# Kernel tuning notes

Measured on AMD Instinct MI355X. Metric: run time of the kernel, lower is better.

Reference implementation:

```python
import jax, jax.numpy as jnp
from jax import lax
import numpy as np

# --- module hyperparams (match S2_GaussianBlur(nr=2048, nc=2048, kernelSize=10, scale=2, RealData=False)) ---
NR, NC, KS, SCALE = 2048, 2048, 10, 2
MTF = np.array([0.38, 0.34, 0.34, 0.26, 0.22, 0.23])  # mtf[[4,5,6,8,10,11]] for scale==2
C = len(MTF)


def _gaussian_kernels():
    # sigmas = scale * sqrt(-2 ln(mtf) / pi^2)
    sigmas = SCALE * np.sqrt(-2.0 * np.log(MTF) / np.pi ** 2)  # (C,)
    end = int(KS / 2) - 0.5
    coords = np.arange(-end, end + 1.0, 1.0)  # (KS,) = [-4.5, ..., 4.5]
    g1 = np.exp(-coords[None, :] ** 2 / (2.0 * sigmas[:, None] ** 2)) / (
        sigmas[:, None] * np.sqrt(2.0 * np.pi))  # (C,KS)
    k = g1[:, :, None] * g1[:, None, :]  # separable outer product -> (C,KS,KS)
    k = k / k.sum(axis=(1, 2), keepdims=True)
    return k.astype(np.float32)


_KERNELS = jnp.asarray(_gaussian_kernels())  # (C,KS,KS), fixed buffers (requires_grad=False)

# Offsets replicating: circular pad by (nr//2, nc//2), conv with full-image kernel B
# (Gaussian patch placed at [row_start:row_end, col_start:col_end], then flipped both
# axes), crop [0:-1, 0:-1].  This collapses exactly to a circular cross-correlation
# with the flipped KSxKS patch at a fixed shift:
_MIDL, _MIDC = NR // 2, NC // 2
_EB = -int(SCALE / 2)
_ROW_START = int(_MIDL - KS / 2 + _EB)
_COL_START = int(_MIDC - KS / 2 + _EB)
_PAD_T = _MIDL + _ROW_START + KS - NR  # left/top circular pad (=4 here)
_PAD_L = _MIDC + _COL_START + KS - NC
assert 0 <= _PAD_T < KS and 0 <= _PAD_L < KS


def setup_inputs() -> dict:
    key = jax.random.key(0)
    x = jax.random.normal(key, (1, C, NR, NC), dtype=jnp.float32)
    return {"x": x}


def _blur(x):
    # circular (wrap) pad so every output pixel sees its KSxKS circular neighborhood
    xpad = jnp.pad(x, ((0, 0), (0, 0), (_PAD_T, KS - 1 - _PAD_T), (_PAD_L, KS - 1 - _PAD_L)), mode="wrap")
    # flipped Gaussian patch (the full-image kernel B was flipped on both axes)
    w = _KERNELS[:, ::-1, ::-1][:, None, :, :]  # (C,1,KS,KS), depthwise
    return lax.conv_general_dilated(
        xpad, w, window_strides=(1, 1), padding="VALID",
        dimension_numbers=("NCHW", "OIHW", "NCHW"), feature_group_count=C)


def reference(x):
    return _blur(x)  # (1,C,NR,NC)
```

## Files before the change

### kernel.cpp

```cpp
#include <hip/hip_runtime.h>
#include <math.h>

constexpr int C   = 6;
constexpr int NR  = 2048;
constexpr int NC  = 2048;
constexpr int KS  = 10;
constexpr int PAD = 4;

constexpr int R    = 32;
constexpr int NIT  = R + KS - 1;
constexpr int CPT  = 4;
constexpr int BW   = 256 * CPT;

__device__ __constant__ float MTFf[C] = {0.38f, 0.34f, 0.34f, 0.26f, 0.22f, 0.23f};

__global__ __launch_bounds__(256, 3)
void s2_blur_ring(const float* __restrict__ x, float* __restrict__ out)
{
    const int t  = threadIdx.x;
    const int c  = blockIdx.z;
    const int r0 = blockIdx.y * R;
    const int jt = blockIdx.x * BW + t * CPT;

    const float* xc = x   + (size_t)c * NR * NC;
    float*       oc = out + (size_t)c * NR * NC;

    float w[KS];
    {
        float mtf    = MTFf[c];
        float sig    = 2.0f * sqrtf(-2.0f * logf(mtf) / (float)(M_PI * M_PI));
        float inv2s2 = 1.0f / (2.0f * sig * sig);
        float s = 0.0f;
        #pragma unroll
        for (int d = 0; d < KS; ++d) {
            float cd = -4.5f + (float)d;
            w[d] = expf(-cd * cd * inv2s2);
            s += w[d];
        }
        #pragma unroll
        for (int d = 0; d < KS; ++d) w[d] /= s;
    }

    const int off0 = (jt - PAD +  0 + NC) & (NC - 1);
    const int off1 = (jt - PAD +  4 + NC) & (NC - 1);
    const int off2 = (jt - PAD +  8 + NC) & (NC - 1);
    const int off3 = (jt - PAD + 12 + NC) & (NC - 1);

    float acc[KS][CPT];
    #pragma unroll
    for (int s = 0; s < KS; ++s)
        #pragma unroll
        for (int q = 0; q < CPT; ++q) acc[s][q] = 0.0f;

    float4 f0, f1, f2, f3;
    {
        const float* rp = xc + (size_t)((r0 - PAD + NR) & (NR - 1)) * NC;
        f0 = *(const float4*)(rp + off0);
        f1 = *(const float4*)(rp + off1);
        f2 = *(const float4*)(rp + off2);
        f3 = *(const float4*)(rp + off3);
    }

    #pragma unroll
    for (int k = 0; k < NIT; ++k) {
        float4 g0, g1, g2, g3;
        if (k + 1 < NIT) {
            const float* rp = xc + (size_t)((r0 - PAD + k + 1) & (NR - 1)) * NC;
            g0 = *(const float4*)(rp + off0);
            g1 = *(const float4*)(rp + off1);
            g2 = *(const float4*)(rp + off2);
            g3 = *(const float4*)(rp + off3);
        }

        const float f[16] = {f0.x, f0.y, f0.z, f0.w,
                             f1.x, f1.y, f1.z, f1.w,
                             f2.x, f2.y, f2.z, f2.w,
                             f3.x, f3.y, f3.z, f3.w};
        float H[CPT];
        #pragma unroll
        for (int q = 0; q < CPT; ++q) {
            float a = 0.0f;
            #pragma unroll
            for (int d = 0; d < KS; ++d) a = fmaf(w[d], f[q + d], a);
            H[q] = a;
        }

        #pragma unroll
        for (int o = 0; o < KS; ++o) {
            const int m = k - o;
            if (m >= 0 && m < R) {
                const int s = m % KS;
                #pragma unroll
                for (int q = 0; q < CPT; ++q)
                    acc[s][q] = fmaf(w[o], H[q], acc[s][q]);
            }
        }

        if (k >= KS - 1) {
            const int m = k - (KS - 1);
            const int s = m % KS;
            float* orow = oc + (size_t)(r0 + m) * NC;
            *(float4*)(orow + jt) = make_float4(acc[s][0], acc[s][1], acc[s][2], acc[s][3]);
            #pragma unroll
            for (int q = 0; q < CPT; ++q) acc[s][q] = 0.0f;
        }

        f0 = g0; f1 = g1; f2 = g2; f3 = g3;
    }
}

extern "C" void kernel_launch(void* const* d_in, const int* in_sizes, int n_in,
                              void* d_out, int out_size, void* d_ws, size_t ws_size,
                              hipStream_t stream) {
    const float* x = (const float*)d_in[0];
    float* out = (float*)d_out;
    dim3 grid(NC / BW, NR / R, C);
    dim3 block(256);
    s2_blur_ring<<<grid, block, 0, stream>>>(x, out);
}
```

Baseline: 183.4 us.

## Stage input rows through LDS with async global_load_lds ring buffer

Replaces the four overlapping per-thread float4 global loads per row with two direct global-to-LDS async loads per lane. Each wave gets its own 4-deep LDS ring of rows, prefetched three rows ahead, and explicit s_waitcnt vmcnt waits gate each read. The loop is fully unrolled with compile-time indices so the wait counts and accumulator slots are constants. The aim is fewer redundant vector-memory instructions and fewer prefetch registers. In exchange it adds LDS traffic, and because vmcnt also counts stores, the hand-counted waits may end up more conservative than intended.

```diff
diff --git a/kernel.cpp b/kernel.cpp
--- a/kernel.cpp
+++ b/kernel.cpp
@@ -7,20 +7,37 @@
 constexpr int KS  = 10;
 constexpr int PAD = 4;
 
-constexpr int R    = 32;
-constexpr int NIT  = R + KS - 1;
-constexpr int CPT  = 4;
-constexpr int BW   = 256 * CPT;
+constexpr int R     = 32;
+constexpr int NIT   = R + KS - 1;
+constexpr int CPT   = 4;
+constexpr int BW    = 256 * CPT;
+constexpr int DEPTH = 4;
+constexpr int WROW  = 272;
 
 __device__ __constant__ float MTFf[C] = {0.38f, 0.34f, 0.34f, 0.26f, 0.22f, 0.23f};
 
+template<int K> struct IC { static constexpr int v = K; };
+template<int K, int N, typename F>
+__device__ __forceinline__ void static_for(F&& f) {
+    if constexpr (K < N) { f(IC<K>{}); static_for<K + 1, N>(f); }
+}
+
+template<int N> __device__ __forceinline__ void vm_wait() {
+    asm volatile("s_waitcnt vmcnt(%0)" :: "n"(N) : "memory");
+}
+
 __global__ __launch_bounds__(256, 3)
-void s2_blur_ring(const float* __restrict__ x, float* __restrict__ out)
+void s2_blur_lds(const float* __restrict__ x, float* __restrict__ out)
 {
-    const int t  = threadIdx.x;
-    const int c  = blockIdx.z;
-    const int r0 = blockIdx.y * R;
-    const int jt = blockIdx.x * BW + t * CPT;
+    __shared__ __align__(16) float lds[4][DEPTH][WROW];
+
+    const int t     = threadIdx.x;
+    const int ln    = t & 63;
+    const int wv    = t >> 6;
+    const int c     = blockIdx.z;
+    const int r0    = blockIdx.y * R;
+    const int jt    = blockIdx.x * BW + t * CPT;
+    const int wbase = blockIdx.x * BW + wv * 256;
 
     const float* xc = x   + (size_t)c * NR * NC;
     float*       oc = out + (size_t)c * NR * NC;
@@ -41,41 +58,43 @@
         for (int d = 0; d < KS; ++d) w[d] /= s;
     }
 
-    const int off0 = (jt - PAD +  0 + NC) & (NC - 1);
-    const int off1 = (jt - PAD +  4 + NC) & (NC - 1);
-    const int off2 = (jt - PAD +  8 + NC) & (NC - 1);
-    const int off3 = (jt - PAD + 12 + NC) & (NC - 1);
+    const int sA = (wbase -  4 + ln * 4 + NC) & (NC - 1);
+    const int sB = (wbase + 12 + ln * 4 + NC) & (NC - 1);
 
-    float acc[KS][CPT];
-    #pragma unroll
-    for (int s = 0; s < KS; ++s)
-        #pragma unroll
-        for (int q = 0; q < CPT; ++q) acc[s][q] = 0.0f;
+    float* lb0 = &lds[wv][0][0];
 
-    float4 f0, f1, f2, f3;
-    {
-        const float* rp = xc + (size_t)((r0 - PAD + NR) & (NR - 1)) * NC;
-        f0 = *(const float4*)(rp + off0);
-        f1 = *(const float4*)(rp + off1);
-        f2 = *(const float4*)(rp + off2);
-        f3 = *(const float4*)(rp + off3);
-    }
+    auto issue = [&](int k) {
+        const float* rp = xc + (size_t)((r0 - PAD + k + NR) & (NR - 1)) * NC;
+        float* lb = lb0 + (k & (DEPTH - 1)) * WROW;
+        __builtin_amdgcn_global_load_lds(
+            (const __attribute__((address_space(1))) void*)(rp + sA),
+            (__attribute__((address_space(3))) void*)(lb), 16, 0, 0);
+        __builtin_amdgcn_global_load_lds(
+            (const __attribute__((address_space(1))) void*)(rp + sB),
+            (__attribute__((address_space(3))) void*)(lb + 16), 16, 0, 0);
+    };
 
-    #pragma unroll
-    for (int k = 0; k < NIT; ++k) {
-        float4 g0, g1, g2, g3;
-        if (k + 1 < NIT) {
-            const float* rp = xc + (size_t)((r0 - PAD + k + 1) & (NR - 1)) * NC;
-            g0 = *(const float4*)(rp + off0);
-            g1 = *(const float4*)(rp + off1);
-            g2 = *(const float4*)(rp + off2);
-            g3 = *(const float4*)(rp + off3);
-        }
+    float acc[KS][CPT] = {};
 
-        const float f[16] = {f0.x, f0.y, f0.z, f0.w,
-                             f1.x, f1.y, f1.z, f1.w,
-                             f2.x, f2.y, f2.z, f2.w,
-                             f3.x, f3.y, f3.z, f3.w};
+    issue(0); issue(1); issue(2);
+
+    static_for<0, NIT>([&](auto ic) {
+        constexpr int k = decltype(ic)::v;
+
+        if constexpr (k + 3 < NIT) issue(k + 3);
+
+        constexpr int rem = NIT - 1 - k;
+        vm_wait<2 * (rem < 3 ? rem : 3)>();
+
+        const float* lb = lb0 + (k & (DEPTH - 1)) * WROW + ln * 4;
+        float4 a0 = *(const float4*)(lb + 0);
+        float4 a1 = *(const float4*)(lb + 4);
+        float4 a2 = *(const float4*)(lb + 8);
+        float4 a3 = *(const float4*)(lb + 12);
+        const float f[16] = {a0.x, a0.y, a0.z, a0.w,
+                             a1.x, a1.y, a1.z, a1.w,
+                             a2.x, a2.y, a2.z, a2.w,
+                             a3.x, a3.y, a3.z, a3.w};
         float H[CPT];
         #pragma unroll
         for (int q = 0; q < CPT; ++q) {
@@ -96,17 +115,15 @@
             }
         }
 
-        if (k >= KS - 1) {
-            const int m = k - (KS - 1);
-            const int s = m % KS;
+        if constexpr (k >= KS - 1) {
+            constexpr int m = k - (KS - 1);
+            constexpr int s = m % KS;
             float* orow = oc + (size_t)(r0 + m) * NC;
             *(float4*)(orow + jt) = make_float4(acc[s][0], acc[s][1], acc[s][2], acc[s][3]);
             #pragma unroll
             for (int q = 0; q < CPT; ++q) acc[s][q] = 0.0f;
         }
-
-        f0 = g0; f1 = g1; f2 = g2; f3 = g3;
-    }
+    });
 }
 
 extern "C" void kernel_launch(void* const* d_in, const int* in_sizes, int n_in,
@@ -116,5 +133,5 @@
     float* out = (float*)d_out;
     dim3 grid(NC / BW, NR / R, C);
     dim3 block(256);
-    s2_blur_ring<<<grid, block, 0, stream>>>(x, out);
+    s2_blur_lds<<<grid, block, 0, stream>>>(x, out);
 }
```

New measurement: 184.5 us. Within noise of the previous version (+0.6%).
